# Optimization experiments

Hardware: AMD Instinct MI355X
Metric: run time of the kernel (lower is better)

The kernel has to match this reference:

```python
import jax, jax.numpy as jnp
import numpy as np

B, N, D_IN = 8, 2048, 1024
H, DH = 4, 256  # num_heads, per-head dim (hidden_dim)
D_OUT = 256


def setup_inputs() -> dict:
    key = jax.random.key(0)
    ks = jax.random.split(key, 5)
    s = 0.02
    return {
        "x": jax.random.normal(ks[0], (B, N, D_IN), dtype=jnp.float32),
        "Wq": jax.random.normal(ks[1], (D_IN, H * DH), dtype=jnp.float32) * s,
        "bq": jnp.zeros((H * DH,), dtype=jnp.float32),
        "Wk": jax.random.normal(ks[2], (D_IN, H * DH), dtype=jnp.float32) * s,
        "bk": jnp.zeros((H * DH,), dtype=jnp.float32),
        "Wv": jax.random.normal(ks[3], (D_IN, H * DH), dtype=jnp.float32) * s,
        "bv": jnp.zeros((H * DH,), dtype=jnp.float32),
        "Wo": jax.random.normal(ks[4], (H * DH, D_OUT), dtype=jnp.float32) * s,
        "bo": jnp.zeros((D_OUT,), dtype=jnp.float32),
    }


def reference(x, Wq, bq, Wk, bk, Wv, bv, Wo, bo):
    b, n, _ = x.shape
    # projections -> [B, N, H, DH]
    q = (x @ Wq + bq).reshape(b, n, H, DH)
    k = (x @ Wk + bk).reshape(b, n, H, DH)
    v = (x @ Wv + bv).reshape(b, n, H, DH)
    scale = 1.0 / jnp.sqrt(jnp.asarray(DH, dtype=x.dtype))
    scores = jnp.einsum("bnhd,bmhd->bhnm", q, k) * scale  # [B,H,N,N]
    weights = jax.nn.softmax(scores, axis=-1)
    attn = jnp.einsum("bhnm,bmhd->bnhd", weights, v)  # [B,N,H,DH]
    attn = attn.reshape(b, n, H * DH)
    return attn @ Wo + bo  # [B, N, D_OUT]
```

## Files before the change

### kernel.cpp

```cpp
#include <hip/hip_runtime.h>
#include <hip/hip_bf16.h>
#include <stdint.h>

typedef __attribute__((ext_vector_type(4))) float  f32x4;
typedef __attribute__((ext_vector_type(4))) float  float4v;
typedef __attribute__((ext_vector_type(8))) short  short8v;
typedef __attribute__((ext_vector_type(4))) short  short4v;
typedef __attribute__((ext_vector_type(8))) unsigned short ushort8v;
typedef __attribute__((ext_vector_type(4))) unsigned short ushort4v;

#define B_   8
#define N_   2048
#define DIN  1024
#define H_   4
#define DH   256
#define QSZ  (B_ * N_ * H_ * DH)

__device__ __forceinline__ unsigned short f2bf(float x) {
  union { float f; unsigned u; } v; v.f = x;
  unsigned r = v.u + 0x7fffu + ((v.u >> 16) & 1u);
  return (unsigned short)(r >> 16);
}

__device__ __forceinline__ short8v pack8(short4v lo, short4v hi) {
  short8v r;
  r[0] = lo[0]; r[1] = lo[1]; r[2] = lo[2]; r[3] = lo[3];
  r[4] = hi[0]; r[5] = hi[1]; r[6] = hi[2]; r[7] = hi[3];
  return r;
}

__device__ __forceinline__ ushort4v ulo4(ushort8v v) {
  ushort4v r; r[0] = v[0]; r[1] = v[1]; r[2] = v[2]; r[3] = v[3]; return r;
}
__device__ __forceinline__ ushort4v uhi4(ushort8v v) {
  ushort4v r; r[0] = v[4]; r[1] = v[5]; r[2] = v[6]; r[3] = v[7]; return r;
}
__device__ __forceinline__ ushort8v umk8(ushort4v a, ushort4v b) {
  ushort8v r;
  r[0] = a[0]; r[1] = a[1]; r[2] = a[2]; r[3] = a[3];
  r[4] = b[0]; r[5] = b[1]; r[6] = b[2]; r[7] = b[3];
  return r;
}

__device__ __forceinline__ void gload_lds16(const void* g, void* l) {
  __builtin_amdgcn_global_load_lds(
      (const __attribute__((address_space(1))) unsigned int*)g,
      (__attribute__((address_space(3))) unsigned int*)l, 16, 0, 0);
}

__global__ __launch_bounds__(256) void prep_wt(
    const float* __restrict__ Wq, const float* __restrict__ Wk,
    const float* __restrict__ Wv, const float* __restrict__ Wo,
    unsigned short* __restrict__ Wt)
{
  __shared__ float Lt[64][68];
  const int tid = threadIdx.x;
  const int c0 = blockIdx.x * 64;
  const int k0 = blockIdx.y * 64;
  const int msel = c0 >> 10;
  const float* src = (msel == 0) ? Wq : (msel == 1) ? Wk : (msel == 2) ? Wv : Wo;
  const int stride = (msel == 3) ? 256 : 1024;
  const int cloc = c0 - msel * 1024;
  #pragma unroll
  for (int p = 0; p < 4; ++p) {
    int kr = p * 16 + (tid >> 4), c4 = (tid & 15) * 4;
    float4v v = *(const float4v*)(src + (size_t)(k0 + kr) * stride + cloc + c4);
    Lt[kr][c4 + 0] = v[0]; Lt[kr][c4 + 1] = v[1];
    Lt[kr][c4 + 2] = v[2]; Lt[kr][c4 + 3] = v[3];
  }
  __syncthreads();
  int n = tid >> 2, kc = (tid & 3) * 16;
  ushort8v h0, h1;
  #pragma unroll
  for (int j = 0; j < 8; ++j) h0[j] = f2bf(Lt[kc + j][n]);
  #pragma unroll
  for (int j = 0; j < 8; ++j) h1[j] = f2bf(Lt[kc + 8 + j][n]);
  unsigned short* dst = Wt + (size_t)(c0 + n) * 1024 + k0 + kc;
  *(ushort8v*)dst = h0;
  *(ushort8v*)(dst + 8) = h1;
}

__global__ __launch_bounds__(512) void qkv_gemm2(
    const float* __restrict__ x, const unsigned short* __restrict__ Wt,
    const float* __restrict__ bq, const float* __restrict__ bk,
    const float* __restrict__ bv, unsigned short* __restrict__ qkv)
{
  __shared__ __align__(16) unsigned short Ab[2][4096];
  __shared__ __align__(16) unsigned short Bb[2][8192];
  const int tid = threadIdx.x;
  const int lane = tid & 63, wid = tid >> 6;
  const int l15 = lane & 15, l4 = lane >> 4;

  const int id = blockIdx.x;
  const int swz = (id & 7) * 192 + (id >> 3);
  const int m0 = (swz / 12) * 128, n0 = (swz % 12) * 256;
  const int wm = (wid >> 2) * 64, wn = (wid & 3) * 64;

  const int arow = tid >> 2, akb = (tid & 3) * 16;
  const int brow1 = wid * 16 + (lane >> 2), bkb = (lane & 3) * 16;
  const float* Abase = x + (size_t)(m0 + arow) * 1024 + (akb >> 1);
  const char* Bg1 = (const char*)Wt + (size_t)(n0 + brow1) * 2048 + bkb;
  const char* Bg2 = Bg1 + 128 * 2048;

  f32x4 acc[4][4] = {};

#define QSTAGE(t, b) do {                                                    \
    float4v f0 = *(const float4v*)(Abase + (t) * 32);                        \
    float4v f1 = *(const float4v*)(Abase + (t) * 32 + 4);                    \
    gload_lds16(Bg1 + (t) * 64, (char*)&Bb[b][0] + wid * 1024);              \
    gload_lds16(Bg2 + (t) * 64, (char*)&Bb[b][0] + 8192 + wid * 1024);       \
    ushort8v hv;                                                             \
    hv[0] = f2bf(f0[0]); hv[1] = f2bf(f0[1]);                                \
    hv[2] = f2bf(f0[2]); hv[3] = f2bf(f0[3]);                                \
    hv[4] = f2bf(f1[0]); hv[5] = f2bf(f1[1]);                                \
    hv[6] = f2bf(f1[2]); hv[7] = f2bf(f1[3]);                                \
    *(ushort8v*)((char*)&Ab[b][0] + tid * 16) = hv;                          \
  } while (0)

  QSTAGE(0, 0);
  __syncthreads();

  for (int t = 0; t < 32; ++t) {
    const int cur = t & 1;
    if (t < 31) QSTAGE(t + 1, cur ^ 1);
    short8v a[4], b[4];
    #pragma unroll
    for (int mf = 0; mf < 4; ++mf)
      a[mf] = *(const short8v*)((const char*)&Ab[cur][0] +
                                (wm + mf * 16 + l15) * 64 + l4 * 16);
    #pragma unroll
    for (int nf = 0; nf < 4; ++nf)
      b[nf] = *(const short8v*)((const char*)&Bb[cur][0] +
                                (wn + nf * 16 + l15) * 64 + l4 * 16);
    #pragma unroll
    for (int mf = 0; mf < 4; ++mf)
      #pragma unroll
      for (int nf = 0; nf < 4; ++nf)
        acc[mf][nf] = __builtin_amdgcn_mfma_f32_16x16x32_bf16(a[mf], b[nf], acc[mf][nf], 0, 0, 0);
    __syncthreads();
  }
#undef QSTAGE

  const int wsel = n0 >> 10;
  const float* bias = (wsel == 0) ? bq : (wsel == 1) ? bk : bv;
  const float scale = (wsel == 0) ? 0.0625f : 1.0f;
  unsigned short* dst = qkv + (size_t)wsel * QSZ;
  #pragma unroll
  for (int nf = 0; nf < 4; ++nf) {
    int ncol = n0 + wn + nf * 16 + l15;
    int ncl = ncol & 1023;
    float bv_ = bias[ncl];
    int h = ncl >> 8, d = ncl & 255;
    #pragma unroll
    for (int mf = 0; mf < 4; ++mf)
      #pragma unroll
      for (int e = 0; e < 4; ++e) {
        int mrow = m0 + wm + mf * 16 + l4 * 4 + e;
        int bb = mrow >> 11, nn = mrow & 2047;
        dst[((size_t)(bb * 4 + h) * 2048 + nn) * 256 + d] =
            f2bf((acc[mf][nf][e] + bv_) * scale);
      }
  }
}

__global__ __launch_bounds__(256) void attn_fused(
    unsigned short* __restrict__ qkv)
{
  __shared__ __align__(16) unsigned short Kbuf[2][8192];
  __shared__ __align__(16) unsigned short Vbuf[2][8192];
  const int tid = threadIdx.x;
  const int lane = tid & 63, wid = tid >> 6;
  const int l15 = lane & 15, l4 = lane >> 4;

  const int id0 = blockIdx.x;
  const int swzb = (id0 & 7) * 64 + (id0 >> 3);
  const int qt = swzb & 15, bh = swzb >> 4;

  const unsigned short* Qh = qkv + (size_t)bh * (N_ * DH);
  const unsigned short* Kh = qkv + (size_t)QSZ + (size_t)bh * (N_ * DH);
  const unsigned short* Vh = qkv + (size_t)2 * QSZ + (size_t)bh * (N_ * DH);

  const int q0 = qt * 128 + wid * 32;
  short8v qf0[8], qf1[8];
  #pragma unroll
  for (int ks = 0; ks < 8; ++ks) {
    const unsigned short* p0 = Qh + (size_t)(q0 + l15) * DH + ks * 32 + l4 * 4;
    const unsigned short* p1 = p0 + 16 * DH;
    qf0[ks] = pack8(*(const short4v*)p0, *(const short4v*)(p0 + 16));
    qf1[ks] = pack8(*(const short4v*)p1, *(const short4v*)(p1 + 16));
  }

  const int skv = tid >> 3, sks = tid & 7;
  const unsigned short* Kg = Kh + (size_t)skv * DH + sks * 32;
  int kdst[4];
  #pragma unroll
  for (int g = 0; g < 4; ++g)
    kdst[g] = (skv * 512 + sks * 64 + g * 16) ^ ((skv & 7) << 4);

  int vgoff[4];
  #pragma unroll
  for (int r = 0; r < 4; ++r)
    vgoff[r] = (lane >> 1) * 512 + (r * 4 + wid) * 32 + (lane & 1) * 16;

  f32x4 ot0[16] = {}, ot1[16] = {};
  float m0r = -1.0e30f, m1r = -1.0e30f, l0r = 0.0f, l1r = 0.0f;

  ushort8v kin0, kin1, kin2, kin3;

#define KISSUE(t) do {                                                       \
    const unsigned short* kp = Kg + (size_t)(t) * (32 * DH);                 \
    kin0 = *(const ushort8v*)(kp);                                           \
    kin1 = *(const ushort8v*)(kp + 8);                                       \
    kin2 = *(const ushort8v*)(kp + 16);                                      \
    kin3 = *(const ushort8v*)(kp + 24);                                      \
  } while (0)

#define KWRITE(b) do {                                                       \
    char* kb = (char*)&Kbuf[b][0];                                           \
    *(ushort8v*)(kb + kdst[0]) = umk8(ulo4(kin0), ulo4(kin2));               \
    *(ushort8v*)(kb + kdst[1]) = umk8(uhi4(kin0), uhi4(kin2));               \
    *(ushort8v*)(kb + kdst[2]) = umk8(ulo4(kin1), ulo4(kin3));               \
    *(ushort8v*)(kb + kdst[3]) = umk8(uhi4(kin1), uhi4(kin3));               \
  } while (0)

#define VISSUE(t, b) do {                                                    \
    const char* vg = (const char*)Vh + (size_t)(t) * 16384;                  \
    _Pragma("unroll")                                                        \
    for (int r = 0; r < 4; ++r)                                              \
      gload_lds16(vg + vgoff[r], (char*)&Vbuf[b][0] + r * 4096 + wid * 1024);\
  } while (0)

#define TR2(d0v, d1v, dfp) do {                                              \
    unsigned ab = vb + (unsigned)(dfp) * 1024u;                              \
    asm volatile("ds_read_b64_tr_b16 %0, %1" : "=v"(d0v) : "v"(ab));         \
    asm volatile("ds_read_b64_tr_b16 %0, %1" : "=v"(d1v) : "v"(ab + 512u));  \
  } while (0)

#define PVG(R0,R1,R2,R3,R4,R5,R6,R7, N0,N1,N2,N3,N4,N5,N6,N7, g, last) do {  \
    if (!(last)) {                                                           \
      TR2(N0, N1, 4 * (g) + 4); TR2(N2, N3, 4 * (g) + 5);                    \
      TR2(N4, N5, 4 * (g) + 6); TR2(N6, N7, 4 * (g) + 7);                    \
      asm volatile("s_waitcnt lgkmcnt(8)" ::: "memory");                     \
    } else {                                                                 \
      asm volatile("s_waitcnt lgkmcnt(0)" ::: "memory");                     \
    }                                                                        \
    __builtin_amdgcn_sched_barrier(0);                                       \
    __builtin_amdgcn_s_setprio(1);                                           \
    ot0[4*(g)+0] = __builtin_amdgcn_mfma_f32_16x16x32_bf16(pack8(R0,R1), pb0, ot0[4*(g)+0], 0,0,0); \
    ot1[4*(g)+0] = __builtin_amdgcn_mfma_f32_16x16x32_bf16(pack8(R0,R1), pb1, ot1[4*(g)+0], 0,0,0); \
    ot0[4*(g)+1] = __builtin_amdgcn_mfma_f32_16x16x32_bf16(pack8(R2,R3), pb0, ot0[4*(g)+1], 0,0,0); \
    ot1[4*(g)+1] = __builtin_amdgcn_mfma_f32_16x16x32_bf16(pack8(R2,R3), pb1, ot1[4*(g)+1], 0,0,0); \
    ot0[4*(g)+2] = __builtin_amdgcn_mfma_f32_16x16x32_bf16(pack8(R4,R5), pb0, ot0[4*(g)+2], 0,0,0); \
    ot1[4*(g)+2] = __builtin_amdgcn_mfma_f32_16x16x32_bf16(pack8(R4,R5), pb1, ot1[4*(g)+2], 0,0,0); \
    ot0[4*(g)+3] = __builtin_amdgcn_mfma_f32_16x16x32_bf16(pack8(R6,R7), pb0, ot0[4*(g)+3], 0,0,0); \
    ot1[4*(g)+3] = __builtin_amdgcn_mfma_f32_16x16x32_bf16(pack8(R6,R7), pb1, ot1[4*(g)+3], 0,0,0); \
    __builtin_amdgcn_s_setprio(0);                                           \
  } while (0)

  KISSUE(0);
  VISSUE(0, 0);
  KWRITE(0);
  __syncthreads();

  for (int t = 0; t < 64; ++t) {
    const int cur = t & 1;
    if (t < 63) { KISSUE(t + 1); VISSUE(t + 1, cur ^ 1); }

    const char* Kc = (const char*)&Kbuf[cur][0];
    const int swzk = (l15 & 7) << 4;
    f32x4 st00 = {0,0,0,0}, st01 = {0,0,0,0}, st10 = {0,0,0,0}, st11 = {0,0,0,0};
    __builtin_amdgcn_s_setprio(1);
    #pragma unroll
    for (int ks = 0; ks < 8; ++ks) {
      int o = (ks * 64 + l4 * 16) ^ swzk;
      short8v af0 = *(const short8v*)(Kc + l15 * 512 + o);
      short8v af1 = *(const short8v*)(Kc + (16 + l15) * 512 + o);
      st00 = __builtin_amdgcn_mfma_f32_16x16x32_bf16(af0, qf0[ks], st00, 0, 0, 0);
      st01 = __builtin_amdgcn_mfma_f32_16x16x32_bf16(af0, qf1[ks], st01, 0, 0, 0);
      st10 = __builtin_amdgcn_mfma_f32_16x16x32_bf16(af1, qf0[ks], st10, 0, 0, 0);
      st11 = __builtin_amdgcn_mfma_f32_16x16x32_bf16(af1, qf1[ks], st11, 0, 0, 0);
    }
    __builtin_amdgcn_s_setprio(0);

    if (t < 63) KWRITE(cur ^ 1);

    short8v pb0, pb1;
    {
      float tmax = fmaxf(fmaxf(st00[0], st00[1]), fmaxf(st00[2], st00[3]));
      tmax = fmaxf(tmax, fmaxf(fmaxf(st10[0], st10[1]), fmaxf(st10[2], st10[3])));
      tmax = fmaxf(tmax, __shfl_xor(tmax, 16));
      tmax = fmaxf(tmax, __shfl_xor(tmax, 32));
      if (__any(tmax > m0r + 8.0f)) {
        float mn = fmaxf(m0r, tmax), al = __expf(m0r - mn);
        l0r *= al;
        #pragma unroll
        for (int df = 0; df < 16; ++df) ot0[df] *= al;
        m0r = mn;
      }
      float psum = 0.0f;
      #pragma unroll
      for (int e = 0; e < 4; ++e) {
        float p0 = __expf(st00[e] - m0r), p1 = __expf(st10[e] - m0r);
        pb0[e] = (short)f2bf(p0); pb0[e + 4] = (short)f2bf(p1);
        psum += p0 + p1;
      }
      psum += __shfl_xor(psum, 16);
      psum += __shfl_xor(psum, 32);
      l0r += psum;
    }
    {
      float tmax = fmaxf(fmaxf(st01[0], st01[1]), fmaxf(st01[2], st01[3]));
      tmax = fmaxf(tmax, fmaxf(fmaxf(st11[0], st11[1]), fmaxf(st11[2], st11[3])));
      tmax = fmaxf(tmax, __shfl_xor(tmax, 16));
      tmax = fmaxf(tmax, __shfl_xor(tmax, 32));
      if (__any(tmax > m1r + 8.0f)) {
        float mn = fmaxf(m1r, tmax), al = __expf(m1r - mn);
        l1r *= al;
        #pragma unroll
        for (int df = 0; df < 16; ++df) ot1[df] *= al;
        m1r = mn;
      }
      float psum = 0.0f;
      #pragma unroll
      for (int e = 0; e < 4; ++e) {
        float p0 = __expf(st01[e] - m1r), p1 = __expf(st11[e] - m1r);
        pb1[e] = (short)f2bf(p0); pb1[e + 4] = (short)f2bf(p1);
        psum += p0 + p1;
      }
      psum += __shfl_xor(psum, 16);
      psum += __shfl_xor(psum, 32);
      l1r += psum;
    }

    const unsigned vb = (unsigned)(uintptr_t)(&Vbuf[cur][0]) + lane * 8;
    short4v A0,A1,A2,A3,A4,A5,A6,A7, B0,B1,B2,B3,B4,B5,B6,B7;
    TR2(A0, A1, 0); TR2(A2, A3, 1); TR2(A4, A5, 2); TR2(A6, A7, 3);
    PVG(A0,A1,A2,A3,A4,A5,A6,A7, B0,B1,B2,B3,B4,B5,B6,B7, 0, 0);
    PVG(B0,B1,B2,B3,B4,B5,B6,B7, A0,A1,A2,A3,A4,A5,A6,A7, 1, 0);
    PVG(A0,A1,A2,A3,A4,A5,A6,A7, B0,B1,B2,B3,B4,B5,B6,B7, 2, 0);
    PVG(B0,B1,B2,B3,B4,B5,B6,B7, A0,A1,A2,A3,A4,A5,A6,A7, 3, 1);

    __syncthreads();
  }

  unsigned short* Oq = (unsigned short*)Qh;
  {
    float inv = 1.0f / l0r;
    size_t base = (size_t)(q0 + l15) * DH;
    #pragma unroll
    for (int df = 0; df < 16; ++df) {
      ushort4v o;
      #pragma unroll
      for (int e = 0; e < 4; ++e) o[e] = f2bf(ot0[df][e] * inv);
      *(ushort4v*)&Oq[base + df * 16 + l4 * 4] = o;
    }
  }
  {
    float inv = 1.0f / l1r;
    size_t base = (size_t)(q0 + 16 + l15) * DH;
    #pragma unroll
    for (int df = 0; df < 16; ++df) {
      ushort4v o;
      #pragma unroll
      for (int e = 0; e < 4; ++e) o[e] = f2bf(ot1[df][e] * inv);
      *(ushort4v*)&Oq[base + df * 16 + l4 * 4] = o;
    }
  }
#undef KISSUE
#undef KWRITE
#undef VISSUE
#undef TR2
#undef PVG
}

__global__ __launch_bounds__(512) void out_gemm2(
    const unsigned short* __restrict__ Aq, const unsigned short* __restrict__ WoT,
    const float* __restrict__ bo, float* __restrict__ out)
{
  __shared__ __align__(16) unsigned short Ab[2][4096];
  __shared__ __align__(16) unsigned short Bb[2][8192];
  const int tid = threadIdx.x;
  const int lane = tid & 63, wid = tid >> 6;
  const int l15 = lane & 15, l4 = lane >> 4;
  const int m0 = blockIdx.x * 128;
  const int wm = (wid >> 2) * 64, wn = (wid & 3) * 64;

  const int arow = wid * 16 + (lane >> 2), akb = (lane & 3) * 16;
  const int bb = m0 >> 11;
  const int qrow = (m0 & 2047) + arow;
  const char* Bg1 = (const char*)WoT + (size_t)arow * 2048 + akb;
  const char* Bg2 = Bg1 + 128 * 2048;

  f32x4 acc[4][4] = {};

#define OSTAGE(t, b) do {                                                    \
    int h = (t) >> 3, d0 = (((t) & 7) * 32) + (akb >> 1);                    \
    gload_lds16(Aq + ((size_t)(bb * 4 + h) * 2048 + qrow) * 256 + d0,        \
                (char*)&Ab[b][0] + wid * 1024);                              \
    gload_lds16(Bg1 + (t) * 64, (char*)&Bb[b][0] + wid * 1024);              \
    gload_lds16(Bg2 + (t) * 64, (char*)&Bb[b][0] + 8192 + wid * 1024);       \
  } while (0)

  OSTAGE(0, 0);
  __syncthreads();

  for (int t = 0; t < 32; ++t) {
    const int cur = t & 1;
    if (t < 31) OSTAGE(t + 1, cur ^ 1);
    short8v a[4], b[4];
    #pragma unroll
    for (int mf = 0; mf < 4; ++mf)
      a[mf] = *(const short8v*)((const char*)&Ab[cur][0] +
                                (wm + mf * 16 + l15) * 64 + l4 * 16);
    #pragma unroll
    for (int nf = 0; nf < 4; ++nf)
      b[nf] = *(const short8v*)((const char*)&Bb[cur][0] +
                                (wn + nf * 16 + l15) * 64 + l4 * 16);
    #pragma unroll
    for (int mf = 0; mf < 4; ++mf)
      #pragma unroll
      for (int nf = 0; nf < 4; ++nf)
        acc[mf][nf] = __builtin_amdgcn_mfma_f32_16x16x32_bf16(a[mf], b[nf], acc[mf][nf], 0, 0, 0);
    __syncthreads();
  }
#undef OSTAGE

  #pragma unroll
  for (int nf = 0; nf < 4; ++nf) {
    int ncol = wn + nf * 16 + l15;
    float bv_ = bo[ncol];
    #pragma unroll
    for (int mf = 0; mf < 4; ++mf)
      #pragma unroll
      for (int e = 0; e < 4; ++e) {
        int mrow = m0 + wm + mf * 16 + l4 * 4 + e;
        out[(size_t)mrow * 256 + ncol] = acc[mf][nf][e] + bv_;
      }
  }
}

extern "C" void kernel_launch(void* const* d_in, const int* in_sizes, int n_in,
                              void* d_out, int out_size, void* d_ws, size_t ws_size,
                              hipStream_t stream) {
  const float* x  = (const float*)d_in[0];
  const float* Wq = (const float*)d_in[1];
  const float* bq = (const float*)d_in[2];
  const float* Wk = (const float*)d_in[3];
  const float* bk = (const float*)d_in[4];
  const float* Wv = (const float*)d_in[5];
  const float* bv = (const float*)d_in[6];
  const float* Wo = (const float*)d_in[7];
  const float* bo = (const float*)d_in[8];

  unsigned short* qkvbuf = (unsigned short*)d_ws;
  unsigned short* Wt     = qkvbuf + (size_t)3 * QSZ;
  float* out = (float*)d_out;

  prep_wt  <<<dim3(52, 16), 256, 0, stream>>>(Wq, Wk, Wv, Wo, Wt);
  qkv_gemm2<<<dim3(1536),   512, 0, stream>>>(x, Wt, bq, bk, bv, qkvbuf);
  attn_fused<<<dim3(512),   256, 0, stream>>>(qkvbuf);
  out_gemm2<<<dim3(128),    512, 0, stream>>>(qkvbuf, Wt + (size_t)3072 * 1024, bo, out);
}
```

Measured before the change: 400.3 us.

## Fold log2e into Q scale, use exp2, and hoist V transposed reads before softmax

```diff
diff --git a/kernel.cpp b/kernel.cpp
--- a/kernel.cpp
+++ b/kernel.cpp
@@ -143,7 +143,7 @@
 
   const int wsel = n0 >> 10;
   const float* bias = (wsel == 0) ? bq : (wsel == 1) ? bk : bv;
-  const float scale = (wsel == 0) ? 0.0625f : 1.0f;
+  const float scale = (wsel == 0) ? 0.0625f * 1.44269504f : 1.0f;
   unsigned short* dst = qkv + (size_t)wsel * QSZ;
   #pragma unroll
   for (int nf = 0; nf < 4; ++nf) {
@@ -236,24 +236,17 @@
     asm volatile("ds_read_b64_tr_b16 %0, %1" : "=v"(d1v) : "v"(ab + 512u));  \
   } while (0)
 
-#define PVG(R0,R1,R2,R3,R4,R5,R6,R7, N0,N1,N2,N3,N4,N5,N6,N7, g, last) do {  \
-    if (!(last)) {                                                           \
-      TR2(N0, N1, 4 * (g) + 4); TR2(N2, N3, 4 * (g) + 5);                    \
-      TR2(N4, N5, 4 * (g) + 6); TR2(N6, N7, 4 * (g) + 7);                    \
-      asm volatile("s_waitcnt lgkmcnt(8)" ::: "memory");                     \
-    } else {                                                                 \
-      asm volatile("s_waitcnt lgkmcnt(0)" ::: "memory");                     \
-    }                                                                        \
-    __builtin_amdgcn_sched_barrier(0);                                       \
+#define PVMFMA(gb, R0,R1,R2,R3,R4,R5,R6,R7)                                  \
+  do {                                                                       \
     __builtin_amdgcn_s_setprio(1);                                           \
-    ot0[4*(g)+0] = __builtin_amdgcn_mfma_f32_16x16x32_bf16(pack8(R0,R1), pb0, ot0[4*(g)+0], 0,0,0); \
-    ot1[4*(g)+0] = __builtin_amdgcn_mfma_f32_16x16x32_bf16(pack8(R0,R1), pb1, ot1[4*(g)+0], 0,0,0); \
-    ot0[4*(g)+1] = __builtin_amdgcn_mfma_f32_16x16x32_bf16(pack8(R2,R3), pb0, ot0[4*(g)+1], 0,0,0); \
-    ot1[4*(g)+1] = __builtin_amdgcn_mfma_f32_16x16x32_bf16(pack8(R2,R3), pb1, ot1[4*(g)+1], 0,0,0); \
-    ot0[4*(g)+2] = __builtin_amdgcn_mfma_f32_16x16x32_bf16(pack8(R4,R5), pb0, ot0[4*(g)+2], 0,0,0); \
-    ot1[4*(g)+2] = __builtin_amdgcn_mfma_f32_16x16x32_bf16(pack8(R4,R5), pb1, ot1[4*(g)+2], 0,0,0); \
-    ot0[4*(g)+3] = __builtin_amdgcn_mfma_f32_16x16x32_bf16(pack8(R6,R7), pb0, ot0[4*(g)+3], 0,0,0); \
-    ot1[4*(g)+3] = __builtin_amdgcn_mfma_f32_16x16x32_bf16(pack8(R6,R7), pb1, ot1[4*(g)+3], 0,0,0); \
+    ot0[(gb)+0] = __builtin_amdgcn_mfma_f32_16x16x32_bf16(pack8(R0,R1), pb0, ot0[(gb)+0], 0,0,0); \
+    ot1[(gb)+0] = __builtin_amdgcn_mfma_f32_16x16x32_bf16(pack8(R0,R1), pb1, ot1[(gb)+0], 0,0,0); \
+    ot0[(gb)+1] = __builtin_amdgcn_mfma_f32_16x16x32_bf16(pack8(R2,R3), pb0, ot0[(gb)+1], 0,0,0); \
+    ot1[(gb)+1] = __builtin_amdgcn_mfma_f32_16x16x32_bf16(pack8(R2,R3), pb1, ot1[(gb)+1], 0,0,0); \
+    ot0[(gb)+2] = __builtin_amdgcn_mfma_f32_16x16x32_bf16(pack8(R4,R5), pb0, ot0[(gb)+2], 0,0,0); \
+    ot1[(gb)+2] = __builtin_amdgcn_mfma_f32_16x16x32_bf16(pack8(R4,R5), pb1, ot1[(gb)+2], 0,0,0); \
+    ot0[(gb)+3] = __builtin_amdgcn_mfma_f32_16x16x32_bf16(pack8(R6,R7), pb0, ot0[(gb)+3], 0,0,0); \
+    ot1[(gb)+3] = __builtin_amdgcn_mfma_f32_16x16x32_bf16(pack8(R6,R7), pb1, ot1[(gb)+3], 0,0,0); \
     __builtin_amdgcn_s_setprio(0);                                           \
   } while (0)
 
@@ -282,63 +275,65 @@
     }
     __builtin_amdgcn_s_setprio(0);
 
+    const unsigned vb = (unsigned)(uintptr_t)(&Vbuf[cur][0]) + lane * 8;
+    short4v A0,A1,A2,A3,A4,A5,A6,A7, B0,B1,B2,B3,B4,B5,B6,B7;
+    TR2(A0, A1, 0); TR2(A2, A3, 1); TR2(A4, A5, 2); TR2(A6, A7, 3);
+    TR2(B0, B1, 4); TR2(B2, B3, 5); TR2(B4, B5, 6); TR2(B6, B7, 7);
+
     if (t < 63) KWRITE(cur ^ 1);
 
     short8v pb0, pb1;
     {
-      float tmax = fmaxf(fmaxf(st00[0], st00[1]), fmaxf(st00[2], st00[3]));
-      tmax = fmaxf(tmax, fmaxf(fmaxf(st10[0], st10[1]), fmaxf(st10[2], st10[3])));
-      tmax = fmaxf(tmax, __shfl_xor(tmax, 16));
-      tmax = fmaxf(tmax, __shfl_xor(tmax, 32));
-      if (__any(tmax > m0r + 8.0f)) {
-        float mn = fmaxf(m0r, tmax), al = __expf(m0r - mn);
+      float tmax0 = fmaxf(fmaxf(fmaxf(st00[0], st00[1]), fmaxf(st00[2], st00[3])),
+                          fmaxf(fmaxf(st10[0], st10[1]), fmaxf(st10[2], st10[3])));
+      float tmax1 = fmaxf(fmaxf(fmaxf(st01[0], st01[1]), fmaxf(st01[2], st01[3])),
+                          fmaxf(fmaxf(st11[0], st11[1]), fmaxf(st11[2], st11[3])));
+      tmax0 = fmaxf(tmax0, __shfl_xor(tmax0, 16));
+      tmax1 = fmaxf(tmax1, __shfl_xor(tmax1, 16));
+      tmax0 = fmaxf(tmax0, __shfl_xor(tmax0, 32));
+      tmax1 = fmaxf(tmax1, __shfl_xor(tmax1, 32));
+      if (__any(tmax0 > m0r + 11.54f)) {
+        float mn = fmaxf(m0r, tmax0), al = exp2f(m0r - mn);
         l0r *= al;
         #pragma unroll
         for (int df = 0; df < 16; ++df) ot0[df] *= al;
         m0r = mn;
       }
-      float psum = 0.0f;
-      #pragma unroll
-      for (int e = 0; e < 4; ++e) {
-        float p0 = __expf(st00[e] - m0r), p1 = __expf(st10[e] - m0r);
-        pb0[e] = (short)f2bf(p0); pb0[e + 4] = (short)f2bf(p1);
-        psum += p0 + p1;
-      }
-      psum += __shfl_xor(psum, 16);
-      psum += __shfl_xor(psum, 32);
-      l0r += psum;
-    }
-    {
-      float tmax = fmaxf(fmaxf(st01[0], st01[1]), fmaxf(st01[2], st01[3]));
-      tmax = fmaxf(tmax, fmaxf(fmaxf(st11[0], st11[1]), fmaxf(st11[2], st11[3])));
-      tmax = fmaxf(tmax, __shfl_xor(tmax, 16));
-      tmax = fmaxf(tmax, __shfl_xor(tmax, 32));
-      if (__any(tmax > m1r + 8.0f)) {
-        float mn = fmaxf(m1r, tmax), al = __expf(m1r - mn);
+      if (__any(tmax1 > m1r + 11.54f)) {
+        float mn = fmaxf(m1r, tmax1), al = exp2f(m1r - mn);
         l1r *= al;
         #pragma unroll
         for (int df = 0; df < 16; ++df) ot1[df] *= al;
         m1r = mn;
       }
-      float psum = 0.0f;
+      float ps0 = 0.0f, ps1 = 0.0f;
       #pragma unroll
       for (int e = 0; e < 4; ++e) {
-        float p0 = __expf(st01[e] - m1r), p1 = __expf(st11[e] - m1r);
-        pb1[e] = (short)f2bf(p0); pb1[e + 4] = (short)f2bf(p1);
-        psum += p0 + p1;
+        float p00 = exp2f(st00[e] - m0r), p10 = exp2f(st10[e] - m0r);
+        float p01 = exp2f(st01[e] - m1r), p11 = exp2f(st11[e] - m1r);
+        pb0[e] = (short)f2bf(p00); pb0[e + 4] = (short)f2bf(p10);
+        pb1[e] = (short)f2bf(p01); pb1[e + 4] = (short)f2bf(p11);
+        ps0 += p00 + p10; ps1 += p01 + p11;
       }
-      psum += __shfl_xor(psum, 16);
-      psum += __shfl_xor(psum, 32);
-      l1r += psum;
+      ps0 += __shfl_xor(ps0, 16);
+      ps1 += __shfl_xor(ps1, 16);
+      ps0 += __shfl_xor(ps0, 32);
+      ps1 += __shfl_xor(ps1, 32);
+      l0r += ps0; l1r += ps1;
     }
 
-    const unsigned vb = (unsigned)(uintptr_t)(&Vbuf[cur][0]) + lane * 8;
-    short4v A0,A1,A2,A3,A4,A5,A6,A7, B0,B1,B2,B3,B4,B5,B6,B7;
-    TR2(A0, A1, 0); TR2(A2, A3, 1); TR2(A4, A5, 2); TR2(A6, A7, 3);
-    PVG(A0,A1,A2,A3,A4,A5,A6,A7, B0,B1,B2,B3,B4,B5,B6,B7, 0, 0);
-    PVG(B0,B1,B2,B3,B4,B5,B6,B7, A0,A1,A2,A3,A4,A5,A6,A7, 1, 0);
-    PVG(A0,A1,A2,A3,A4,A5,A6,A7, B0,B1,B2,B3,B4,B5,B6,B7, 2, 0);
-    PVG(B0,B1,B2,B3,B4,B5,B6,B7, A0,A1,A2,A3,A4,A5,A6,A7, 3, 1);
+    asm volatile("s_waitcnt lgkmcnt(0)" ::: "memory");
+    __builtin_amdgcn_sched_barrier(0);
+    PVMFMA(0, A0,A1,A2,A3,A4,A5,A6,A7);
+    TR2(A0, A1, 8); TR2(A2, A3, 9); TR2(A4, A5, 10); TR2(A6, A7, 11);
+    PVMFMA(4, B0,B1,B2,B3,B4,B5,B6,B7);
+    TR2(B0, B1, 12); TR2(B2, B3, 13); TR2(B4, B5, 14); TR2(B6, B7, 15);
+    asm volatile("s_waitcnt lgkmcnt(8)" ::: "memory");
+    __builtin_amdgcn_sched_barrier(0);
+    PVMFMA(8, A0,A1,A2,A3,A4,A5,A6,A7);
+    asm volatile("s_waitcnt lgkmcnt(0)" ::: "memory");
+    __builtin_amdgcn_sched_barrier(0);
+    PVMFMA(12, B0,B1,B2,B3,B4,B5,B6,B7);
 
     __syncthreads();
   }
@@ -370,7 +365,7 @@
 #undef KWRITE
 #undef VISSUE
 #undef TR2
-#undef PVG
+#undef PVMFMA
 }
 
 __global__ __launch_bounds__(512) void out_gemm2(
```

Result: slower. 417.7 us (+4.3%).
